# Performance work log

Hardware: AMD Instinct MI355X
Metric: run time of the kernel (lower is better)

The kernel has to match this reference:

```python
import jax, jax.numpy as jnp
import numpy as np

N = 4096          # number of cells
M = 8             # number of morphogen channels
FOUR_PI = 4.0 * np.pi
EPS = 1e-8


def setup_inputs() -> dict:
    key = jax.random.key(0)
    k1, k2, k3, k4 = jax.random.split(key, 4)
    position = jax.random.uniform(k1, (N, 3), dtype=jnp.float32) * 100.0   # cells in a 100^3 box
    radius = 0.5 + jax.random.uniform(k2, (N,), dtype=jnp.float32) * 0.5   # cell radii in [0.5, 1.0]
    secretion = jax.random.uniform(k3, (N, M), dtype=jnp.float32)          # per-cell source strengths
    active = jax.random.randint(k4, (N,), 0, 2) > 0                        # bool mask on source cells
    diffusion_coefs = jnp.asarray([0.5, 1.0, 2.0, 4.0, 0.25, 1.5, 3.0, 0.75], dtype=jnp.float32)
    degradation_rates = jnp.asarray([0.01, 0.02, 0.005, 0.04, 0.01, 0.03, 0.008, 0.02], dtype=jnp.float32)
    return {
        "position": position,
        "radius": radius,
        "secretion": secretion,
        "diffusion_coefs": diffusion_coefs,
        "degradation_rates": degradation_rates,
        "active": active,
    }


def reference(position, radius, secretion, diffusion_coefs, degradation_rates, active):
    # Pairwise distances [N, N]; clamp below by source-cell radius to avoid the
    # 1/r singularity at the self term (field evaluated at the cell surface).
    diff = position[:, None, :] - position[None, :, :]            # [N, N, 3]
    dist = jnp.sqrt(jnp.sum(diff * diff, axis=-1) + EPS)          # [N, N]
    dist = jnp.maximum(dist, radius[None, :])                     # clamp by source radius

    # Steady-state 3D diffusion-degradation Green's function per morphogen m:
    #   G_m(r) = exp(-r / lambda_m) / (4 pi D_m r),  lambda_m = sqrt(D_m / k_m)
    lam = jnp.sqrt(diffusion_coefs / degradation_rates)           # [M]
    d = dist[:, :, None]                                          # [N, N, 1]
    kernel = jnp.exp(-d / lam) / (FOUR_PI * diffusion_coefs * d)  # [N, N, M]

    # Only active cells secrete.
    src = secretion * active[:, None].astype(secretion.dtype)     # [N, M]
    concentrations = jnp.einsum("ijm,jm->im", kernel, src)        # [N, M]
    return concentrations
```

## Files before the change

### kernel.cpp

```cpp
#include <hip/hip_runtime.h>
#include <math.h>

#define NN 4096
#define MM 8
#define BLOCK 256
#define JT 64
#define FOUR_PI_F 12.566370614359172f
#define EPS_F 1e-8f
#define LOG2E_F 1.4426950408889634f


template <bool DUP015>
__device__ __forceinline__ void run_tile(
    int nact, const float4* __restrict__ sj, const float4* __restrict__ ss,
    float px, float py, float pz, const float* __restrict__ na,
    float* __restrict__ acc)
{
#pragma unroll 4
    for (int jj = 0; jj < nact; ++jj) {
        const float4 pj = sj[jj];
        const float4 s0 = ss[jj * 2 + 0];
        const float4 s1 = ss[jj * 2 + 1];
        float dx = px - pj.x;
        float dy = py - pj.y;
        float dz = pz - pj.z;
        float d2 = fmaf(dx, dx, fmaf(dy, dy, fmaf(dz, dz, EPS_F)));
        float d2c = fmaxf(d2, pj.w);
        float rs = __builtin_amdgcn_rsqf(d2c);
        float dcl = d2c * rs;

        float ers[MM];
        if constexpr (DUP015) {
            float eA = __builtin_amdgcn_exp2f(dcl * na[0]) * rs;
            ers[0] = eA; ers[1] = eA; ers[5] = eA;
            ers[2] = __builtin_amdgcn_exp2f(dcl * na[2]) * rs;
            ers[3] = __builtin_amdgcn_exp2f(dcl * na[3]) * rs;
            ers[4] = __builtin_amdgcn_exp2f(dcl * na[4]) * rs;
            ers[6] = __builtin_amdgcn_exp2f(dcl * na[6]) * rs;
            ers[7] = __builtin_amdgcn_exp2f(dcl * na[7]) * rs;
        } else {
#pragma unroll
            for (int m = 0; m < MM; ++m)
                ers[m] = __builtin_amdgcn_exp2f(dcl * na[m]) * rs;
        }

        const float s[MM] = {s0.x, s0.y, s0.z, s0.w, s1.x, s1.y, s1.z, s1.w};
#pragma unroll
        for (int m = 0; m < MM; ++m)
            acc[m] = fmaf(ers[m], s[m], acc[m]);
    }
}

__global__ __launch_bounds__(BLOCK) void diff_partial(
    const float* __restrict__ pos,
    const float* __restrict__ radius,
    const float* __restrict__ secretion,
    const float* __restrict__ Dc,
    const float* __restrict__ Kd,
    const int*   __restrict__ active,
    float* __restrict__ partial,
    int jrange)
{
    __shared__ float4 sj[JT];
    __shared__ float4 ss[JT * 2];
    __shared__ int s_nact;

    const int tid = threadIdx.x;
    const int i = blockIdx.x * BLOCK + tid;
    const int j0base = blockIdx.y * jrange;

    float na[MM], invD[MM], acc[MM];
#pragma unroll
    for (int m = 0; m < MM; ++m) {
        float lam = sqrtf(Dc[m] / Kd[m]);
        na[m] = -LOG2E_F / lam;
        invD[m] = 1.0f / (FOUR_PI_F * Dc[m]);
        acc[m] = 0.0f;
    }
    const bool dup015 = (na[0] == na[1]) && (na[0] == na[5]);

    const float px = pos[i * 3 + 0];
    const float py = pos[i * 3 + 1];
    const float pz = pos[i * 3 + 2];

    for (int t = 0; t < jrange; t += JT) {
        const int j0 = j0base + t;
        __syncthreads();

        if (tid < JT) {
            const int j = j0 + tid;
            const bool act = (active[j] != 0);
            const unsigned long long mask = __ballot(act);
            if (tid == 0) s_nact = __popcll(mask);
            if (act) {
                const int k = __popcll(mask & ((1ull << tid) - 1ull));
                const float r = radius[j];
                sj[k] = make_float4(pos[j * 3 + 0], pos[j * 3 + 1],
                                    pos[j * 3 + 2], r * r);
                const float4 s0 =
                    reinterpret_cast<const float4*>(secretion)[j * 2 + 0];
                const float4 s1 =
                    reinterpret_cast<const float4*>(secretion)[j * 2 + 1];
                ss[k * 2 + 0] = make_float4(s0.x * invD[0], s0.y * invD[1],
                                            s0.z * invD[2], s0.w * invD[3]);
                ss[k * 2 + 1] = make_float4(s1.x * invD[4], s1.y * invD[5],
                                            s1.z * invD[6], s1.w * invD[7]);
            }
        }
        __syncthreads();

        const int nact = s_nact;
        if (dup015)
            run_tile<true>(nact, sj, ss, px, py, pz, na, acc);
        else
            run_tile<false>(nact, sj, ss, px, py, pz, na, acc);
    }

    float4* dst = reinterpret_cast<float4*>(
        partial + (size_t)blockIdx.y * NN * MM + (size_t)i * MM);
    dst[0] = make_float4(acc[0], acc[1], acc[2], acc[3]);
    dst[1] = make_float4(acc[4], acc[5], acc[6], acc[7]);
}

__global__ __launch_bounds__(BLOCK) void diff_reduce(
    const float4* __restrict__ partial, float4* __restrict__ out, int C)
{
    int idx = blockIdx.x * BLOCK + threadIdx.x;
    float4 s = make_float4(0.f, 0.f, 0.f, 0.f);
    for (int c = 0; c < C; ++c) {
        float4 p = partial[(size_t)c * (NN * MM / 4) + idx];
        s.x += p.x; s.y += p.y; s.z += p.z; s.w += p.w;
    }
    out[idx] = s;
}

extern "C" void kernel_launch(void* const* d_in, const int* in_sizes, int n_in,
                              void* d_out, int out_size, void* d_ws, size_t ws_size,
                              hipStream_t stream) {
    const float* pos       = (const float*)d_in[0];
    const float* radius    = (const float*)d_in[1];
    const float* secretion = (const float*)d_in[2];
    const float* Dc        = (const float*)d_in[3];
    const float* Kd        = (const float*)d_in[4];
    const int*   active    = (const int*)d_in[5];
    float* out = (float*)d_out;

    const size_t slice = (size_t)NN * MM * sizeof(float);

    int C = 64;
    while (C > 1 && (size_t)C * slice > ws_size) C >>= 1;

    if ((size_t)C * slice <= ws_size) {
        float* partial = (float*)d_ws;
        int jrange = NN / C;
        dim3 grid(NN / BLOCK, C);
        diff_partial<<<grid, BLOCK, 0, stream>>>(pos, radius, secretion, Dc, Kd,
                                                 active, partial, jrange);
        diff_reduce<<<(NN * MM / 4 + BLOCK - 1) / BLOCK, BLOCK, 0, stream>>>(
            (const float4*)partial, (float4*)out, C);
    } else {
        dim3 grid(NN / BLOCK, 1);
        diff_partial<<<grid, BLOCK, 0, stream>>>(pos, radius, secretion, Dc, Kd,
                                                 active, out, NN);
    }
}
```

Before: 95.63 us.

## Replace partial-sum workspace and reduce kernel with atomic accumulation

Removes the separate reduction kernel and per-chunk partial buffer. Each block now atomically adds its per-cell accumulators straight into the output, which is zeroed first with a memset. The j-split drops from 64 chunks to 32, so there are fewer blocks but each does more work. This saves a kernel launch and the partial-buffer traffic, at the cost of atomic contention, an extra memset, and a non-deterministic summation order.

```diff
diff --git a/kernel.cpp b/kernel.cpp
--- a/kernel.cpp
+++ b/kernel.cpp
@@ -5,6 +5,7 @@
 #define MM 8
 #define BLOCK 256
 #define JT 64
+#define CCHUNK 32
 #define FOUR_PI_F 12.566370614359172f
 #define EPS_F 1e-8f
 #define LOG2E_F 1.4426950408889634f
@@ -51,14 +52,14 @@
     }
 }
 
-__global__ __launch_bounds__(BLOCK) void diff_partial(
+__global__ __launch_bounds__(BLOCK) void diff_fused(
     const float* __restrict__ pos,
     const float* __restrict__ radius,
     const float* __restrict__ secretion,
     const float* __restrict__ Dc,
     const float* __restrict__ Kd,
     const int*   __restrict__ active,
-    float* __restrict__ partial,
+    float* out,
     int jrange)
 {
     __shared__ float4 sj[JT];
@@ -116,22 +117,10 @@
             run_tile<false>(nact, sj, ss, px, py, pz, na, acc);
     }
 
-    float4* dst = reinterpret_cast<float4*>(
-        partial + (size_t)blockIdx.y * NN * MM + (size_t)i * MM);
-    dst[0] = make_float4(acc[0], acc[1], acc[2], acc[3]);
-    dst[1] = make_float4(acc[4], acc[5], acc[6], acc[7]);
-}
-
-__global__ __launch_bounds__(BLOCK) void diff_reduce(
-    const float4* __restrict__ partial, float4* __restrict__ out, int C)
-{
-    int idx = blockIdx.x * BLOCK + threadIdx.x;
-    float4 s = make_float4(0.f, 0.f, 0.f, 0.f);
-    for (int c = 0; c < C; ++c) {
-        float4 p = partial[(size_t)c * (NN * MM / 4) + idx];
-        s.x += p.x; s.y += p.y; s.z += p.z; s.w += p.w;
-    }
-    out[idx] = s;
+    float* dst = out + (size_t)i * MM;
+#pragma unroll
+    for (int m = 0; m < MM; ++m)
+        unsafeAtomicAdd(dst + m, acc[m]);
 }
 
 extern "C" void kernel_launch(void* const* d_in, const int* in_sizes, int n_in,
@@ -145,22 +134,9 @@
     const int*   active    = (const int*)d_in[5];
     float* out = (float*)d_out;
 
-    const size_t slice = (size_t)NN * MM * sizeof(float);
+    hipMemsetAsync(out, 0, (size_t)NN * MM * sizeof(float), stream);
 
-    int C = 64;
-    while (C > 1 && (size_t)C * slice > ws_size) C >>= 1;
-
-    if ((size_t)C * slice <= ws_size) {
-        float* partial = (float*)d_ws;
-        int jrange = NN / C;
-        dim3 grid(NN / BLOCK, C);
-        diff_partial<<<grid, BLOCK, 0, stream>>>(pos, radius, secretion, Dc, Kd,
-                                                 active, partial, jrange);
-        diff_reduce<<<(NN * MM / 4 + BLOCK - 1) / BLOCK, BLOCK, 0, stream>>>(
-            (const float4*)partial, (float4*)out, C);
-    } else {
-        dim3 grid(NN / BLOCK, 1);
-        diff_partial<<<grid, BLOCK, 0, stream>>>(pos, radius, secretion, Dc, Kd,
-                                                 active, out, NN);
-    }
+    dim3 grid(NN / BLOCK, CCHUNK);
+    diff_fused<<<grid, BLOCK, 0, stream>>>(pos, radius, secretion, Dc, Kd,
+                                           active, out, NN / CCHUNK);
 }
```

New measurement: 106.3 us. 11.1% more time.

## Derive exps by squaring, process two cells per thread, and parallelize reduction

Applied to the files above, without the earlier changes.

When the decay rates form a doubling chain, checked at runtime with a tolerance, two of the six exponentials per pair are replaced by squaring a previous exponential. Each thread now accumulates two target cells, so every source tile loaded into shared memory is reused twice. The source range is split into 128 chunks of one 32-source tile each, and the reduce kernel splits the chunk sum across four thread groups combined through shared memory. The aim is fewer transcendental ops per pair, less per-pair LDS traffic, and more parallelism. In exchange it adds register pressure, a larger partial buffer, slight rounding differences from squaring, and drops the fallback path used when the workspace is too small.

```diff
diff --git a/kernel.cpp b/kernel.cpp
--- a/kernel.cpp
+++ b/kernel.cpp
@@ -4,87 +4,109 @@
 #define NN 4096
 #define MM 8
 #define BLOCK 256
-#define JT 64
+#define IPT 2
+#define IBLK (BLOCK * IPT)
+#define CC 128
+#define JT 32
 #define FOUR_PI_F 12.566370614359172f
 #define EPS_F 1e-8f
 #define LOG2E_F 1.4426950408889634f
 
 
-template <bool DUP015>
+template <int VAR>
 __device__ __forceinline__ void run_tile(
     int nact, const float4* __restrict__ sj, const float4* __restrict__ ss,
-    float px, float py, float pz, const float* __restrict__ na,
-    float* __restrict__ acc)
+    const float* __restrict__ px, const float* __restrict__ py,
+    const float* __restrict__ pz, const float* __restrict__ na,
+    float acc[IPT][MM])
 {
-#pragma unroll 4
+#pragma unroll 2
     for (int jj = 0; jj < nact; ++jj) {
         const float4 pj = sj[jj];
         const float4 s0 = ss[jj * 2 + 0];
         const float4 s1 = ss[jj * 2 + 1];
-        float dx = px - pj.x;
-        float dy = py - pj.y;
-        float dz = pz - pj.z;
-        float d2 = fmaf(dx, dx, fmaf(dy, dy, fmaf(dz, dz, EPS_F)));
-        float d2c = fmaxf(d2, pj.w);
-        float rs = __builtin_amdgcn_rsqf(d2c);
-        float dcl = d2c * rs;
+#pragma unroll
+        for (int r = 0; r < IPT; ++r) {
+            float dx = px[r] - pj.x;
+            float dy = py[r] - pj.y;
+            float dz = pz[r] - pj.z;
+            float d2 = fmaf(dx, dx, fmaf(dy, dy, fmaf(dz, dz, EPS_F)));
+            float d2c = fmaxf(d2, pj.w);
+            float rs = __builtin_amdgcn_rsqf(d2c);
+            float dcl = d2c * rs;
 
-        float ers[MM];
-        if constexpr (DUP015) {
-            float eA = __builtin_amdgcn_exp2f(dcl * na[0]) * rs;
-            ers[0] = eA; ers[1] = eA; ers[5] = eA;
-            ers[2] = __builtin_amdgcn_exp2f(dcl * na[2]) * rs;
-            ers[3] = __builtin_amdgcn_exp2f(dcl * na[3]) * rs;
-            ers[4] = __builtin_amdgcn_exp2f(dcl * na[4]) * rs;
-            ers[6] = __builtin_amdgcn_exp2f(dcl * na[6]) * rs;
-            ers[7] = __builtin_amdgcn_exp2f(dcl * na[7]) * rs;
-        } else {
+            float f[MM];
+            if constexpr (VAR == 2) {
+                float eA = __builtin_amdgcn_exp2f(dcl * na[0]);
+                float e2 = __builtin_amdgcn_exp2f(dcl * na[2]);
+                float e3 = e2 * e2;
+                float e4 = e3 * e3;
+                float e6 = __builtin_amdgcn_exp2f(dcl * na[6]);
+                float e7 = __builtin_amdgcn_exp2f(dcl * na[7]);
+                float fA = eA * rs;
+                f[0] = fA; f[1] = fA; f[5] = fA;
+                f[2] = e2 * rs; f[3] = e3 * rs; f[4] = e4 * rs;
+                f[6] = e6 * rs; f[7] = e7 * rs;
+            } else if constexpr (VAR == 1) {
+                float fA = __builtin_amdgcn_exp2f(dcl * na[0]) * rs;
+                f[0] = fA; f[1] = fA; f[5] = fA;
+                f[2] = __builtin_amdgcn_exp2f(dcl * na[2]) * rs;
+                f[3] = __builtin_amdgcn_exp2f(dcl * na[3]) * rs;
+                f[4] = __builtin_amdgcn_exp2f(dcl * na[4]) * rs;
+                f[6] = __builtin_amdgcn_exp2f(dcl * na[6]) * rs;
+                f[7] = __builtin_amdgcn_exp2f(dcl * na[7]) * rs;
+            } else {
+#pragma unroll
+                for (int m = 0; m < MM; ++m)
+                    f[m] = __builtin_amdgcn_exp2f(dcl * na[m]) * rs;
+            }
+
+            const float s[MM] = {s0.x, s0.y, s0.z, s0.w,
+                                 s1.x, s1.y, s1.z, s1.w};
 #pragma unroll
             for (int m = 0; m < MM; ++m)
-                ers[m] = __builtin_amdgcn_exp2f(dcl * na[m]) * rs;
+                acc[r][m] = fmaf(f[m], s[m], acc[r][m]);
         }
-
-        const float s[MM] = {s0.x, s0.y, s0.z, s0.w, s1.x, s1.y, s1.z, s1.w};
-#pragma unroll
-        for (int m = 0; m < MM; ++m)
-            acc[m] = fmaf(ers[m], s[m], acc[m]);
     }
 }
 
 __global__ __launch_bounds__(BLOCK) void diff_partial(
-    const float* __restrict__ pos,
-    const float* __restrict__ radius,
-    const float* __restrict__ secretion,
-    const float* __restrict__ Dc,
-    const float* __restrict__ Kd,
-    const int*   __restrict__ active,
+    const float* __restrict__ pos, const float* __restrict__ radius,
+    const float* __restrict__ secretion, const float* __restrict__ Dc,
+    const float* __restrict__ Kd, const int* __restrict__ active,
     float* __restrict__ partial,
-    int jrange)
+    int ntiles)
 {
     __shared__ float4 sj[JT];
     __shared__ float4 ss[JT * 2];
     __shared__ int s_nact;
 
     const int tid = threadIdx.x;
-    const int i = blockIdx.x * BLOCK + tid;
-    const int j0base = blockIdx.y * jrange;
+    const int i0 = blockIdx.x * IBLK + tid;
+    const int i1 = i0 + BLOCK;
+    const int j0base = blockIdx.y * (JT * ntiles);
 
-    float na[MM], invD[MM], acc[MM];
+    float na[MM], invD[MM];
+    float acc[IPT][MM];
 #pragma unroll
     for (int m = 0; m < MM; ++m) {
         float lam = sqrtf(Dc[m] / Kd[m]);
         na[m] = -LOG2E_F / lam;
         invD[m] = 1.0f / (FOUR_PI_F * Dc[m]);
-        acc[m] = 0.0f;
+        acc[0][m] = 0.0f; acc[1][m] = 0.0f;
     }
     const bool dup015 = (na[0] == na[1]) && (na[0] == na[5]);
+    const bool chain =
+        dup015 &&
+        (fabsf(na[3] - 2.0f * na[2]) <= 4e-6f * fabsf(na[3])) &&
+        (fabsf(na[4] - 2.0f * na[3]) <= 4e-6f * fabsf(na[4]));
 
-    const float px = pos[i * 3 + 0];
-    const float py = pos[i * 3 + 1];
-    const float pz = pos[i * 3 + 2];
+    const float px[IPT] = {pos[i0 * 3 + 0], pos[i1 * 3 + 0]};
+    const float py[IPT] = {pos[i0 * 3 + 1], pos[i1 * 3 + 1]};
+    const float pz[IPT] = {pos[i0 * 3 + 2], pos[i1 * 3 + 2]};
 
-    for (int t = 0; t < jrange; t += JT) {
-        const int j0 = j0base + t;
+    for (int t = 0; t < ntiles; ++t) {
+        const int j0 = j0base + t * JT;
         __syncthreads();
 
         if (tid < JT) {
@@ -110,28 +132,43 @@
         __syncthreads();
 
         const int nact = s_nact;
-        if (dup015)
-            run_tile<true>(nact, sj, ss, px, py, pz, na, acc);
-        else
-            run_tile<false>(nact, sj, ss, px, py, pz, na, acc);
+        if (chain)       run_tile<2>(nact, sj, ss, px, py, pz, na, acc);
+        else if (dup015) run_tile<1>(nact, sj, ss, px, py, pz, na, acc);
+        else             run_tile<0>(nact, sj, ss, px, py, pz, na, acc);
     }
 
-    float4* dst = reinterpret_cast<float4*>(
-        partial + (size_t)blockIdx.y * NN * MM + (size_t)i * MM);
-    dst[0] = make_float4(acc[0], acc[1], acc[2], acc[3]);
-    dst[1] = make_float4(acc[4], acc[5], acc[6], acc[7]);
+    float* base = partial + (size_t)blockIdx.y * NN * MM;
+    float4* d0 = reinterpret_cast<float4*>(base + (size_t)i0 * MM);
+    float4* d1 = reinterpret_cast<float4*>(base + (size_t)i1 * MM);
+    d0[0] = make_float4(acc[0][0], acc[0][1], acc[0][2], acc[0][3]);
+    d0[1] = make_float4(acc[0][4], acc[0][5], acc[0][6], acc[0][7]);
+    d1[0] = make_float4(acc[1][0], acc[1][1], acc[1][2], acc[1][3]);
+    d1[1] = make_float4(acc[1][4], acc[1][5], acc[1][6], acc[1][7]);
 }
 
 __global__ __launch_bounds__(BLOCK) void diff_reduce(
     const float4* __restrict__ partial, float4* __restrict__ out, int C)
 {
-    int idx = blockIdx.x * BLOCK + threadIdx.x;
+    __shared__ float4 red[4][64];
+    const int tx = threadIdx.x & 63;
+    const int ty = threadIdx.x >> 6;
+    const int o = blockIdx.x * 64 + tx;
+
     float4 s = make_float4(0.f, 0.f, 0.f, 0.f);
-    for (int c = 0; c < C; ++c) {
-        float4 p = partial[(size_t)c * (NN * MM / 4) + idx];
+    for (int c = ty; c < C; c += 4) {
+        const float4 p = partial[(size_t)c * (NN * MM / 4) + o];
         s.x += p.x; s.y += p.y; s.z += p.z; s.w += p.w;
     }
-    out[idx] = s;
+    red[ty][tx] = s;
+    __syncthreads();
+    if (ty == 0) {
+        const float4 a = red[1][tx], b = red[2][tx], c4 = red[3][tx];
+        s.x += a.x + b.x + c4.x;
+        s.y += a.y + b.y + c4.y;
+        s.z += a.z + b.z + c4.z;
+        s.w += a.w + b.w + c4.w;
+        out[o] = s;
+    }
 }
 
 extern "C" void kernel_launch(void* const* d_in, const int* in_sizes, int n_in,
@@ -147,20 +184,14 @@
 
     const size_t slice = (size_t)NN * MM * sizeof(float);
 
-    int C = 64;
-    while (C > 1 && (size_t)C * slice > ws_size) C >>= 1;
+    int C = CC;
+    while (C > 4 && (size_t)C * slice > ws_size) C >>= 1;
+    const int ntiles = NN / (C * JT);
 
-    if ((size_t)C * slice <= ws_size) {
-        float* partial = (float*)d_ws;
-        int jrange = NN / C;
-        dim3 grid(NN / BLOCK, C);
-        diff_partial<<<grid, BLOCK, 0, stream>>>(pos, radius, secretion, Dc, Kd,
-                                                 active, partial, jrange);
-        diff_reduce<<<(NN * MM / 4 + BLOCK - 1) / BLOCK, BLOCK, 0, stream>>>(
-            (const float4*)partial, (float4*)out, C);
-    } else {
-        dim3 grid(NN / BLOCK, 1);
-        diff_partial<<<grid, BLOCK, 0, stream>>>(pos, radius, secretion, Dc, Kd,
-                                                 active, out, NN);
-    }
+    float* partial = (float*)d_ws;
+    dim3 grid(NN / IBLK, C);
+    diff_partial<<<grid, BLOCK, 0, stream>>>(pos, radius, secretion, Dc, Kd,
+                                             active, partial, ntiles);
+    diff_reduce<<<NN * MM / 4 / 64, BLOCK, 0, stream>>>(
+        (const float4*)partial, (float4*)out, C);
 }
```

Result: faster. 90.77 us (-5.1%).
